# Performance work log

Measured on AMD Instinct MI355X. Metric: run time of the kernel, lower is better.

Reference implementation:

```python
import jax, jax.numpy as jnp
import numpy as np

D_MODEL = 1024
D_INNER = 2048   # expand=2
D_STATE = 16
D_CONV = 4
DT_RANK = 64     # ceil(d_model/16)
BATCH = 4
SEQLEN = 2048


def setup_inputs() -> dict:
    key = jax.random.key(0)
    ks = jax.random.split(key, 9)
    f = lambda k, shape, s=0.02: jax.random.normal(k, shape, dtype=jnp.float32) * s
    return {
        "x": jax.random.normal(ks[0], (BATCH, SEQLEN, D_MODEL), dtype=jnp.float32),
        "norm_w": jnp.ones((D_MODEL,), jnp.float32),
        "in_proj_w": f(ks[1], (2 * D_INNER, D_MODEL)),
        "conv_w": f(ks[2], (D_INNER, D_CONV), 0.1),
        "conv_b": f(ks[3], (D_INNER,), 0.1),
        "x_proj_w": f(ks[4], (DT_RANK + 2 * D_STATE, D_INNER)),
        "dt_proj_w": f(ks[5], (D_INNER, DT_RANK), 0.1),
        "dt_proj_b": f(ks[6], (D_INNER,), 0.1),
        "A_log": jnp.log(jnp.tile(jnp.arange(1, D_STATE + 1, dtype=jnp.float32), (D_INNER, 1))),
        "D_param": jnp.ones((D_INNER,), jnp.float32),
        "out_proj_w": f(ks[7], (D_MODEL, D_INNER)),
    }


def _rmsnorm(x, w):
    eps = jnp.finfo(jnp.float32).eps
    var = jnp.mean(x * x, axis=-1, keepdims=True)
    return x * jax.lax.rsqrt(var + eps) * w


def _mamba(x_norm, in_proj_w, conv_w, conv_b, x_proj_w,
           dt_proj_w, dt_proj_b, A_log, D_param, out_proj_w):
    B, L, _ = x_norm.shape
    # input projection -> [B, L, 2*D_INNER], split into x and gate z
    xz = jnp.einsum('bld,ed->ble', x_norm, in_proj_w)
    x_in, z = jnp.split(xz, 2, axis=-1)
    # causal depthwise conv1d (kernel D_CONV, left pad D_CONV-1)
    x_c = jax.lax.conv_general_dilated(
        x_in.transpose(0, 2, 1),                 # [B, D_INNER, L]
        conv_w[:, None, :],                      # [D_INNER, 1, D_CONV]
        window_strides=(1,), padding=[(D_CONV - 1, 0)],
        dimension_numbers=('NCH', 'OIH', 'NCH'),
        feature_group_count=D_INNER,
    ) + conv_b[None, :, None]
    u = jax.nn.silu(x_c.transpose(0, 2, 1))      # [B, L, D_INNER]
    # SSM parameters
    x_dbl = jnp.einsum('bld,ed->ble', u, x_proj_w)  # [B, L, DT_RANK+2*D_STATE]
    dt, B_mat, C_mat = jnp.split(x_dbl, [DT_RANK, DT_RANK + D_STATE], axis=-1)
    dt = jax.nn.softplus(jnp.einsum('blr,dr->bld', dt, dt_proj_w) + dt_proj_b)  # [B,L,D_INNER]
    A = -jnp.exp(A_log)                          # [D_INNER, D_STATE]

    # selective scan over time; state h: [B, D_INNER, D_STATE]
    def step(h, inputs):
        dt_t, B_t, C_t, u_t = inputs             # [B,Dn],[B,S],[B,S],[B,Dn]
        dA = jnp.exp(dt_t[:, :, None] * A)       # [B, Dn, S]
        h = dA * h + (dt_t * u_t)[:, :, None] * B_t[:, None, :]
        y_t = jnp.einsum('bds,bs->bd', h, C_t)
        return h, y_t

    h0 = jnp.zeros((B, D_INNER, D_STATE), x_norm.dtype)
    xs = (dt.transpose(1, 0, 2), B_mat.transpose(1, 0, 2),
          C_mat.transpose(1, 0, 2), u.transpose(1, 0, 2))
    _, ys = jax.lax.scan(step, h0, xs)           # [L, B, D_INNER]
    y = ys.transpose(1, 0, 2) + D_param * u
    y = y * jax.nn.silu(z)
    return jnp.einsum('bld,ed->ble', y, out_proj_w)  # [B, L, D_MODEL]


def reference(x, norm_w, in_proj_w, conv_w, conv_b, x_proj_w,
              dt_proj_w, dt_proj_b, A_log, D_param, out_proj_w):
    x_norm = _rmsnorm(x, norm_w)
    out = _mamba(x_norm, in_proj_w, conv_w, conv_b, x_proj_w,
                 dt_proj_w, dt_proj_b, A_log, D_param, out_proj_w)
    return x + out
```

## Files before the change

kernel.cpp:

```cpp
#include <hip/hip_runtime.h>
#include <hip/hip_bf16.h>
#include <math.h>

#define DM 1024
#define DI 2048
#define DS 16
#define DC 4
#define DR 64
#define NB 4
#define SL 2048
#define BL (NB * SL)
#define DXP (DR + 2 * DS)
#define NC 32
#define CL (SL / NC)

typedef __hip_bfloat16 bf16;
typedef __attribute__((ext_vector_type(8))) short short8;
typedef __attribute__((ext_vector_type(4))) float floatx4;
typedef unsigned int u32;

__device__ __forceinline__ float to_f(float v) { return v; }
__device__ __forceinline__ float to_f(bf16 v) { return __bfloat162float(v); }
template <typename T> __device__ __forceinline__ T from_f(float v);
template <> __device__ __forceinline__ float from_f<float>(float v) { return v; }
template <> __device__ __forceinline__ bf16 from_f<bf16>(float v) { return __float2bfloat16(v); }

__device__ __forceinline__ float bfbits2f(unsigned short u) {
  u32 b = ((u32)u) << 16;
  return __builtin_bit_cast(float, b);
}
__device__ __forceinline__ short f2bfbits(float v) {
  bf16 b = __float2bfloat16(v);
  return __builtin_bit_cast(short, b);
}
__device__ __forceinline__ float fsilu(float v) {
  return v * __builtin_amdgcn_rcpf(1.f + __expf(-v));
}

__device__ __forceinline__ void gload16(const ushort* g, ushort* l) {
  __builtin_amdgcn_global_load_lds((const __attribute__((address_space(1))) void*)g,
                                   (__attribute__((address_space(3))) void*)l,
                                   16, 0, 0);
}

__device__ __forceinline__ void vmw4() { asm volatile("s_waitcnt vmcnt(4)" ::: "memory"); }
__device__ __forceinline__ void vmw0() { asm volatile("s_waitcnt vmcnt(0)" ::: "memory"); }
__device__ __forceinline__ void barx() {
  asm volatile("" ::: "memory");
  __builtin_amdgcn_s_barrier();
  asm volatile("" ::: "memory");
}

__global__ __launch_bounds__(256) void f2b_k(const float* __restrict__ src,
                                             bf16* __restrict__ dst, int n) {
  int i = blockIdx.x * 256 + threadIdx.x;
  if (i < n) dst[i] = from_f<bf16>(src[i]);
}

__global__ __launch_bounds__(256) void rmsnorm_k(const float* __restrict__ x,
                                                 const float* __restrict__ w,
                                                 bf16* __restrict__ o) {
  int row = blockIdx.x;
  const float* xr = x + (size_t)row * DM;
  float ss = 0.f;
  for (int i = threadIdx.x; i < DM; i += 256) { float v = xr[i]; ss += v * v; }
  for (int off = 32; off > 0; off >>= 1) ss += __shfl_down(ss, off);
  __shared__ float sred[4];
  __shared__ float sscale;
  if ((threadIdx.x & 63) == 0) sred[threadIdx.x >> 6] = ss;
  __syncthreads();
  if (threadIdx.x == 0) {
    float t = sred[0] + sred[1] + sred[2] + sred[3];
    sscale = rsqrtf(t / (float)DM + 1.1920929e-7f);
  }
  __syncthreads();
  float sc = sscale;
  bf16* orow = o + (size_t)row * DM;
  for (int i = threadIdx.x; i < DM; i += 256) orow[i] = from_f<bf16>(xr[i] * sc * w[i]);
}

template <int MODE>
__global__ __launch_bounds__(512, 1) void gemm256(const bf16* __restrict__ A,
                                                  const bf16* __restrict__ W,
                                                  int M, int N, int K,
                                                  bf16* __restrict__ Cx,
                                                  bf16* __restrict__ Cz, int nsplit,
                                                  float* __restrict__ Cf,
                                                  const float* __restrict__ R) {
  __shared__ ushort SH[65536];
  const int tid = threadIdx.x;
  const int lane = tid & 63, wv = tid >> 6;
  const int wr = wv >> 2, wc = wv & 3;
  const int row15 = lane & 15, quad = lane >> 4;

  int ntm = M >> 8, ntn = N >> 8, nwg = ntm * ntn;
  int bid = blockIdx.x;
  int swz = (bid & 7) * (nwg >> 3) + (bid >> 3);
  int bm0 = (swz % ntm) << 8, bn0 = (swz / ntm) << 8;

  const int nt = K >> 6;
  const ushort* Au = (const ushort*)A;
  const ushort* Wu = (const ushort*)W;

  const int w4u = lane ^ (((lane >> 5) & 1) << 1);
  const int Wsw = (((row15 << 6) | (quad << 4)) ^ (((row15 >> 3) & 1) << 5));
  const char* SHb = (const char*)SH;
  const int Abase0 = (wr << 14) + Wsw;
  const int Abase1 = 32768 + (wr << 14) + Wsw;
  const int Bbase0 = 65536 + ((wc >> 1) << 14) + ((wc & 1) << 13) + Wsw;
  const int Bbase1 = Bbase0 + 32768;

  auto stageA = [&](int tt, int half, int buf) {
    const ushort* g = Au + (size_t)(bm0 + half * 128) * K + tt * 64;
    char* lds = (char*)SH + (size_t)(buf * 2 + half) * 16384;
#pragma unroll
    for (int i = 0; i < 2; ++i) {
      int sub = wv + i * 8;
      int r = ((sub >> 1) << 4) | (w4u >> 2);
      int ce = ((sub & 1) << 5) | ((w4u & 3) << 3);
      gload16(g + (size_t)r * K + ce, (ushort*)(lds + sub * 1024));
    }
  };
  auto stageB = [&](int tt, int half, int buf) {
    const ushort* g = Wu + (size_t)(bn0 + half * 128) * K + tt * 64;
    char* lds = (char*)SH + 65536 + (size_t)(buf * 2 + half) * 16384;
#pragma unroll
    for (int i = 0; i < 2; ++i) {
      int sub = wv + i * 8;
      int r = ((sub >> 1) << 4) | (w4u >> 2);
      int ce = ((sub & 1) << 5) | ((w4u & 3) << 3);
      gload16(g + (size_t)r * K + ce, (ushort*)(lds + sub * 1024));
    }
  };

  short8 a_f[4][2], bq[2][2][2];
  floatx4 acc[8][4] = {};

#define LDA_(base, mh) do { _Pragma("unroll") for (int mi = 0; mi < 4; ++mi) \
  { _Pragma("unroll") for (int kk = 0; kk < 2; ++kk) \
    a_f[mi][kk] = *(const short8*)(SHb + (base) + ((((mh)*4 + mi)*2 + kk) << 10)); } } while (0)
#define LDB_(base, nh) do { _Pragma("unroll") for (int ni = 0; ni < 2; ++ni) \
  { _Pragma("unroll") for (int kk = 0; kk < 2; ++kk) \
    bq[nh][ni][kk] = *(const short8*)(SHb + (base) + (((((nh)*2 + ni)*2 + kk)) << 10)); } } while (0)
#define MM_(mh, nh) do { __builtin_amdgcn_s_setprio(1); \
  _Pragma("unroll") for (int mi = 0; mi < 4; ++mi) \
  { _Pragma("unroll") for (int ni = 0; ni < 2; ++ni) \
    { _Pragma("unroll") for (int kk = 0; kk < 2; ++kk) \
      acc[(mh)*4+mi][(nh)*2+ni] = __builtin_amdgcn_mfma_f32_16x16x32_bf16( \
          a_f[mi][kk], bq[nh][ni][kk], acc[(mh)*4+mi][(nh)*2+ni], 0, 0, 0); } } \
  __builtin_amdgcn_s_setprio(0); } while (0)

#define TILE_(t, AB, BB, curbuf, nxtbuf) do { \
  int tp1 = (t) + 1, tp2 = (t) + 2; \
  LDA_(AB, 0); LDB_(BB, 0); \
  if (tp1 < nt) stageA(tp1, 0, nxtbuf); \
  barx(); MM_(0, 0); barx(); \
  LDB_(BB, 1); \
  if (tp1 < nt) stageA(tp1, 1, nxtbuf); \
  barx(); MM_(0, 1); barx(); \
  LDA_(AB, 1); \
  if (tp2 < nt) stageB(tp2, 0, curbuf); \
  barx(); MM_(1, 1); barx(); \
  if (tp2 < nt) stageB(tp2, 1, curbuf); \
  barx(); MM_(1, 0); \
  if (tp2 < nt) vmw4(); else vmw0(); \
  barx(); \
} while (0)

  stageB(0, 0, 0); stageB(0, 1, 0); stageA(0, 0, 0); stageA(0, 1, 0);
  stageB(1, 0, 1); stageB(1, 1, 1);
  vmw4();
  barx();

  for (int t = 0; t < nt; t += 2) {
    TILE_(t, Abase0, Bbase0, 0, 1);
    TILE_(t + 1, Abase1, Bbase1, 1, 0);
  }
#undef TILE_
#undef MM_
#undef LDB_
#undef LDA_

#pragma unroll
  for (int mi8 = 0; mi8 < 8; ++mi8) {
#pragma unroll
    for (int ni4 = 0; ni4 < 4; ++ni4) {
#pragma unroll
      for (int reg = 0; reg < 4; ++reg) {
        int grow = bm0 + wr * 128 + mi8 * 16 + quad * 4 + reg;
        int gcol = bn0 + wc * 64 + ni4 * 16 + row15;
        float v = acc[mi8][ni4][reg];
        if (MODE == 1) {
          if (gcol < nsplit) {
            Cx[(size_t)grow * DI + gcol] = from_f<bf16>(v);
          } else {
            Cz[(size_t)grow * DI + (gcol - nsplit)] = from_f<bf16>(fsilu(v));
          }
        } else {
          size_t o = (size_t)grow * N + gcol;
          Cf[o] = v + R[o];
        }
      }
    }
  }
}

#define TM 128
#define TN 128
#define TK 32
#define LDK 40
template <int MODE>
__global__ __launch_bounds__(256) void gemm_mfma(const bf16* __restrict__ A,
                                                 const bf16* __restrict__ W,
                                                 int M, int N, int K,
                                                 bf16* __restrict__ Cx,
                                                 bf16* __restrict__ Cz, int nsplit,
                                                 float* __restrict__ Cf,
                                                 const float* __restrict__ R,
                                                 const float* __restrict__ bias) {
  __shared__ ushort Asm[TM][TK];
  __shared__ ushort Bsm[TN][TK];
  int bm = blockIdx.y * TM, bn = blockIdx.x * TN;
  int tid = threadIdx.x;
  int lane = tid & 63, wave = tid >> 6;
  int wm = (wave & 1) * 64, wn = (wave >> 1) * 64;
  int row15 = lane & 15, quad = lane >> 4;

  int srow = lane >> 2;
  int scol = (lane & 3) * 8;
  int s0 = wave * 2, s1 = wave * 2 + 1;

  const ushort* Au = (const ushort*)A;
  const ushort* Wu = (const ushort*)W;
  const ushort* ag0 = Au + (size_t)(bm + s0 * 16 + srow) * K + scol;
  const ushort* ag1 = Au + (size_t)(bm + s1 * 16 + srow) * K + scol;
  const ushort* bg0 = Wu + (size_t)(bn + s0 * 16 + srow) * K + scol;
  const ushort* bg1 = Wu + (size_t)(bn + s1 * 16 + srow) * K + scol;
  ushort* la0 = &Asm[s0 * 16][0];
  ushort* la1 = &Asm[s1 * 16][0];
  ushort* lb0 = &Bsm[s0 * 16][0];
  ushort* lb1 = &Bsm[s1 * 16][0];

  floatx4 acc[4][4] = {};

  for (int k0 = 0; k0 < K; k0 += TK) {
    gload16(ag0 + k0, la0);
    gload16(ag1 + k0, la1);
    gload16(bg0 + k0, lb0);
    gload16(bg1 + k0, lb1);
    __syncthreads();
    short8 a_f[4], b_f[4];
#pragma unroll
    for (int i = 0; i < 4; ++i)
      a_f[i] = *(const short8*)&Asm[wm + i * 16 + row15][quad * 8];
#pragma unroll
    for (int j = 0; j < 4; ++j)
      b_f[j] = *(const short8*)&Bsm[wn + j * 16 + row15][quad * 8];
#pragma unroll
    for (int i = 0; i < 4; ++i)
#pragma unroll
      for (int j = 0; j < 4; ++j)
        acc[i][j] = __builtin_amdgcn_mfma_f32_16x16x32_bf16(a_f[i], b_f[j], acc[i][j], 0, 0, 0);
    __syncthreads();
  }
#pragma unroll
  for (int mi = 0; mi < 4; ++mi) {
#pragma unroll
    for (int ni = 0; ni < 4; ++ni) {
#pragma unroll
      for (int reg = 0; reg < 4; ++reg) {
        int grow = bm + wm + mi * 16 + quad * 4 + reg;
        int gcol = bn + wn + ni * 16 + row15;
        float v = acc[mi][ni][reg];
        if (MODE == 1) {
          if (gcol < nsplit) {
            Cx[(size_t)grow * DI + gcol] = from_f<bf16>(v);
          } else {
            Cz[(size_t)grow * DI + (gcol - nsplit)] = from_f<bf16>(fsilu(v));
          }
        } else if (MODE == 2) {
          size_t o = (size_t)grow * N + gcol;
          Cf[o] = v + R[o];
        } else {
          float t = v + bias[gcol];
          float sp = (t > 20.f) ? t : __logf(1.f + __expf(t));
          Cx[(size_t)grow * N + gcol] = from_f<bf16>(sp);
        }
      }
    }
  }
}

#define XKS 128
__global__ __launch_bounds__(256) void xproj_k(const bf16* __restrict__ u,
                                               const bf16* __restrict__ w,
                                               float* __restrict__ xdbl) {
  __shared__ ushort Asm[128][LDK];
  __shared__ ushort Bsm[96][LDK];
  int kbase = blockIdx.x * XKS;
  int bm = blockIdx.y * 128;
  int tid = threadIdx.x;
  int lane = tid & 63, wave = tid >> 6;
  int row15 = lane & 15, quad = lane >> 4;
  int srow = tid >> 1, skoff = (tid & 1) * 16;

  floatx4 acc[2][6] = {};
  const ushort* Au = (const ushort*)u;
  const ushort* Wu = (const ushort*)w;
  for (int k0 = kbase; k0 < kbase + XKS; k0 += TK) {
    const ushort* ag = Au + (size_t)(bm + srow) * DI + k0 + skoff;
    *(short8*)&Asm[srow][skoff]     = *(const short8*)ag;
    *(short8*)&Asm[srow][skoff + 8] = *(const short8*)(ag + 8);
    if (tid < 192) {
      const ushort* wg = Wu + (size_t)srow * DI + k0 + skoff;
      *(short8*)&Bsm[srow][skoff]     = *(const short8*)wg;
      *(short8*)&Bsm[srow][skoff + 8] = *(const short8*)(wg + 8);
    }
    __syncthreads();
    short8 a_f[2], b_f[6];
#pragma unroll
    for (int i = 0; i < 2; ++i)
      a_f[i] = *(const short8*)&Asm[wave * 32 + i * 16 + row15][quad * 8];
#pragma unroll
    for (int j = 0; j < 6; ++j)
      b_f[j] = *(const short8*)&Bsm[j * 16 + row15][quad * 8];
#pragma unroll
    for (int i = 0; i < 2; ++i)
#pragma unroll
      for (int j = 0; j < 6; ++j)
        acc[i][j] = __builtin_amdgcn_mfma_f32_16x16x32_bf16(a_f[i], b_f[j], acc[i][j], 0, 0, 0);
    __syncthreads();
  }
#pragma unroll
  for (int mi = 0; mi < 2; ++mi)
#pragma unroll
    for (int nj = 0; nj < 6; ++nj)
#pragma unroll
      for (int reg = 0; reg < 4; ++reg) {
        int grow = bm + wave * 32 + mi * 16 + quad * 4 + reg;
        int gcol = nj * 16 + row15;
        atomicAdd(&xdbl[(size_t)grow * DXP + gcol], acc[mi][nj][reg]);
      }
}

__global__ __launch_bounds__(256) void dtex_k(const float* __restrict__ xdbl,
                                              bf16* __restrict__ dtin) {
  int i = blockIdx.x * 256 + threadIdx.x;
  int r = i >> 6, c = i & 63;
  dtin[i] = from_f<bf16>(xdbl[(size_t)r * DXP + c]);
}

#define TSTRIP 8
__global__ __launch_bounds__(256) void conv_silu_k(const bf16* __restrict__ xin,
                                                   const float* __restrict__ cw,
                                                   const float* __restrict__ cb,
                                                   bf16* __restrict__ u) {
  int blk = blockIdx.x;
  int b = blk >> 8;
  int l0 = (blk & 255) * TSTRIP;
  int c0 = threadIdx.x * 8;

  float4 cw4[8];
  const float4* cwp = (const float4*)cw;
#pragma unroll
  for (int j = 0; j < 8; ++j) cw4[j] = cwp[c0 + j];
  float cbv[8];
  {
    float4 cb0 = *(const float4*)&cb[c0];
    float4 cb1 = *(const float4*)&cb[c0 + 4];
    cbv[0] = cb0.x; cbv[1] = cb0.y; cbv[2] = cb0.z; cbv[3] = cb0.w;
    cbv[4] = cb1.x; cbv[5] = cb1.y; cbv[6] = cb1.z; cbv[7] = cb1.w;
  }

  const ushort* base = (const ushort*)xin + ((size_t)(b * SL + l0) * DI + c0);
  ushort* ubase = (ushort*)u + ((size_t)(b * SL + l0) * DI + c0);

  short8 zz = {};
  short8 w0 = zz, w1 = zz, w2 = zz;
  if (l0 >= 3) {
    w0 = *(const short8*)(base - 3 * DI);
    w1 = *(const short8*)(base - 2 * DI);
    w2 = *(const short8*)(base - 1 * DI);
  }
#pragma unroll
  for (int l = 0; l < TSTRIP; ++l) {
    short8 w3 = *(const short8*)(base + (ptrdiff_t)l * DI);
    short8 outv;
#pragma unroll
    for (int j = 0; j < 8; ++j) {
      float a = cbv[j]
              + bfbits2f((unsigned short)w0[j]) * cw4[j].x
              + bfbits2f((unsigned short)w1[j]) * cw4[j].y
              + bfbits2f((unsigned short)w2[j]) * cw4[j].z
              + bfbits2f((unsigned short)w3[j]) * cw4[j].w;
      outv[j] = f2bfbits(fsilu(a));
    }
    *(short8*)(ubase + (ptrdiff_t)l * DI) = outv;
    w0 = w1; w1 = w2; w2 = w3;
  }
}

__global__ __launch_bounds__(256) void scan_p1(const bf16* __restrict__ dts,
                                               const bf16* __restrict__ u,
                                               const float* __restrict__ xdbl,
                                               const float* __restrict__ A_log,
                                               float* __restrict__ Pbuf,
                                               float* __restrict__ Qbuf) {
  int bid = blockIdx.x;
  int b = bid >> 8;
  int c = (bid >> 3) & (NC - 1);
  int d = (bid & 7) * 256 + threadIdx.x;

  float A[DS], h[DS], P[DS];
#pragma unroll
  for (int s = 0; s < DS; ++s) {
    A[s] = -__expf(A_log[d * DS + s]);
    h[s] = 0.f; P[s] = 1.f;
  }
  size_t bl0 = (size_t)b * SL + c * CL;
  size_t base = bl0 * DI + d;
  size_t xb = bl0 * DXP + DR;
  for (int l = 0; l < CL; ++l) {
    float dtv = to_f(dts[base]);
    float uv = to_f(u[base]);
    float du = dtv * uv;
#pragma unroll
    for (int s = 0; s < DS; ++s) {
      float Bv = xdbl[xb + s];
      float dA = __expf(dtv * A[s]);
      h[s] = dA * h[s] + du * Bv;
      P[s] *= dA;
    }
    base += DI;
    xb += DXP;
  }
  size_t o = ((size_t)(b * NC + c) * DS) * DI + d;
#pragma unroll
  for (int s = 0; s < DS; ++s) {
    Pbuf[o + (size_t)s * DI] = P[s];
    Qbuf[o + (size_t)s * DI] = h[s];
  }
}

__global__ __launch_bounds__(256) void scan_p2(float* __restrict__ Pbuf,
                                               float* __restrict__ Qbuf) {
  int bid = blockIdx.x;
  int b = bid >> 7;
  int s = (bid >> 3) & (DS - 1);
  int d = (bid & 7) * 256 + threadIdx.x;
  float h = 0.f;
  for (int c = 0; c < NC; ++c) {
    size_t idx = ((size_t)((b * NC + c) * DS + s)) * DI + d;
    float Pv = Pbuf[idx];
    float qv = Qbuf[idx];
    Qbuf[idx] = h;
    h = Pv * h + qv;
  }
}

__global__ __launch_bounds__(256) void scan_p3(const bf16* __restrict__ dts,
                                               bf16* __restrict__ u,
                                               const float* __restrict__ xdbl,
                                               const float* __restrict__ A_log,
                                               const float* __restrict__ Dp,
                                               const bf16* __restrict__ g,
                                               const float* __restrict__ Qbuf) {
  int bid = blockIdx.x;
  int b = bid >> 8;
  int c = (bid >> 3) & (NC - 1);
  int d = (bid & 7) * 256 + threadIdx.x;

  float A[DS], h[DS];
  size_t o = ((size_t)(b * NC + c) * DS) * DI + d;
#pragma unroll
  for (int s = 0; s < DS; ++s) {
    A[s] = -__expf(A_log[d * DS + s]);
    h[s] = Qbuf[o + (size_t)s * DI];
  }
  float Dd = Dp[d];
  size_t bl0 = (size_t)b * SL + c * CL;
  size_t base = bl0 * DI + d;
  size_t xb = bl0 * DXP + DR;
  for (int l = 0; l < CL; ++l) {
    float dtv = to_f(dts[base]);
    float uv = to_f(u[base]);
    float gv = to_f(g[base]);
    float du = dtv * uv;
    float p0 = 0.f, p1 = 0.f, p2 = 0.f, p3 = 0.f;
#pragma unroll
    for (int s = 0; s < DS; s += 4) {
      float dA0 = __expf(dtv * A[s + 0]);
      float dA1 = __expf(dtv * A[s + 1]);
      float dA2 = __expf(dtv * A[s + 2]);
      float dA3 = __expf(dtv * A[s + 3]);
      h[s + 0] = dA0 * h[s + 0] + du * xdbl[xb + s + 0];
      h[s + 1] = dA1 * h[s + 1] + du * xdbl[xb + s + 1];
      h[s + 2] = dA2 * h[s + 2] + du * xdbl[xb + s + 2];
      h[s + 3] = dA3 * h[s + 3] + du * xdbl[xb + s + 3];
      p0 += h[s + 0] * xdbl[xb + DS + s + 0];
      p1 += h[s + 1] * xdbl[xb + DS + s + 1];
      p2 += h[s + 2] * xdbl[xb + DS + s + 2];
      p3 += h[s + 3] * xdbl[xb + DS + s + 3];
    }
    float yv = ((p0 + p1) + (p2 + p3)) + Dd * uv;
    u[base] = from_f<bf16>(yv * gv);
    base += DI;
    xb += DXP;
  }
}

extern "C" void kernel_launch(void* const* d_in, const int* in_sizes, int n_in,
                              void* d_out, int out_size, void* d_ws, size_t ws_size,
                              hipStream_t stream) {
  const float* x        = (const float*)d_in[0];
  const float* norm_w   = (const float*)d_in[1];
  const float* in_projw = (const float*)d_in[2];
  const float* conv_w   = (const float*)d_in[3];
  const float* conv_b   = (const float*)d_in[4];
  const float* x_projw  = (const float*)d_in[5];
  const float* dt_projw = (const float*)d_in[6];
  const float* dt_projb = (const float*)d_in[7];
  const float* A_log    = (const float*)d_in[8];
  const float* Dp       = (const float*)d_in[9];
  const float* out_projw= (const float*)d_in[10];
  float* out = (float*)d_out;

  char* wsb = (char*)d_ws;
  bf16* x_buf  = (bf16*)wsb;
  bf16* z_buf  = (bf16*)(wsb + (size_t)BL * DI * 2);
  bf16* u_buf  = (bf16*)(wsb + (size_t)BL * DI * 4);
  char* ovl    = wsb + (size_t)BL * DI * 6;
  bf16* ipw_bf = (bf16*)ovl;
  float* xdbl   = (float*)ovl;
  bf16*  xpw_bf = (bf16*)(ovl + 3145728);
  bf16*  dtw_bf = (bf16*)(ovl + 3538944);
  bf16*  dtin_bf= (bf16*)(ovl + 3801088);
  bf16* xnorm_bf = u_buf;
  bf16* dt_buf   = x_buf;
  bf16* opw_bf   = x_buf;
  float* Pbuf = out;
  float* Qbuf = out + (size_t)NB * NC * DS * DI;

  f2b_k<<<(2 * DI * DM) / 256, 256, 0, stream>>>(in_projw, ipw_bf, 2 * DI * DM);
  rmsnorm_k<<<BL, 256, 0, stream>>>(x, norm_w, xnorm_bf);
  gemm256<1><<<(BL / 256) * (2 * DI / 256), 512, 0, stream>>>(
      xnorm_bf, ipw_bf, BL, 2 * DI, DM, x_buf, z_buf, DI, nullptr, nullptr);
  conv_silu_k<<<NB * (SL / TSTRIP), 256, 0, stream>>>(x_buf, conv_w, conv_b, u_buf);
  hipMemsetAsync(xdbl, 0, (size_t)BL * DXP * sizeof(float), stream);
  f2b_k<<<(DXP * DI + 255) / 256, 256, 0, stream>>>(x_projw, xpw_bf, DXP * DI);
  f2b_k<<<(DI * DR) / 256, 256, 0, stream>>>(dt_projw, dtw_bf, DI * DR);
  xproj_k<<<dim3(DI / XKS, BL / 128), 256, 0, stream>>>(u_buf, xpw_bf, xdbl);
  dtex_k<<<(BL * DR) / 256, 256, 0, stream>>>(xdbl, dtin_bf);
  gemm_mfma<3><<<dim3(DI / TN, BL / TM), 256, 0, stream>>>(
      dtin_bf, dtw_bf, BL, DI, DR, dt_buf, nullptr, 0, nullptr, nullptr, dt_projb);
  scan_p1<<<NB * NC * (DI / 256), 256, 0, stream>>>(dt_buf, u_buf, xdbl, A_log, Pbuf, Qbuf);
  scan_p2<<<NB * DS * (DI / 256), 256, 0, stream>>>(Pbuf, Qbuf);
  scan_p3<<<NB * NC * (DI / 256), 256, 0, stream>>>(dt_buf, u_buf, xdbl, A_log, Dp, z_buf, Qbuf);
  f2b_k<<<(DM * DI) / 256, 256, 0, stream>>>(out_projw, opw_bf, DM * DI);
  gemm256<2><<<(BL / 256) * (DM / 256), 512, 0, stream>>>(
      u_buf, opw_bf, BL, DM, DI, nullptr, nullptr, 0, out, x);
}
```

Baseline: 489.2 us.

## Add 256x128 ping-pong pipelined MFMA GEMM for output projection

Adds a new GEMM kernel with 256x128 tiles, K-step 64, and double-buffered LDS loaded through global_load_lds. MFMA work is interleaved with LDS fragment loads and raises wave priority during MFMA. The out_proj GEMM now uses it in place of the 256x256 kernel. The grid doubles, which raises CU occupancy for the M=8192, N=1024 shape, at the cost of reading the A operand more often and more barriers per tile.

```diff
diff --git a/kernel.cpp b/kernel.cpp
--- a/kernel.cpp
+++ b/kernel.cpp
@@ -44,6 +44,7 @@
 }
 
 __device__ __forceinline__ void vmw4() { asm volatile("s_waitcnt vmcnt(4)" ::: "memory"); }
+__device__ __forceinline__ void vmw2() { asm volatile("s_waitcnt vmcnt(2)" ::: "memory"); }
 __device__ __forceinline__ void vmw0() { asm volatile("s_waitcnt vmcnt(0)" ::: "memory"); }
 __device__ __forceinline__ void barx() {
   asm volatile("" ::: "memory");
@@ -198,6 +199,130 @@
           }
         } else {
           size_t o = (size_t)grow * N + gcol;
+          Cf[o] = v + R[o];
+        }
+      }
+    }
+  }
+}
+
+template <int MODE>
+__global__ __launch_bounds__(512, 1) void gemm_np(const bf16* __restrict__ A,
+                                                  const bf16* __restrict__ W,
+                                                  int M, int N, int K,
+                                                  bf16* __restrict__ Cx,
+                                                  bf16* __restrict__ Cz, int nsplit,
+                                                  float* __restrict__ Cf,
+                                                  const float* __restrict__ R) {
+  __shared__ ushort SH[49152];
+  const int tid = threadIdx.x;
+  const int lane = tid & 63, wv = tid >> 6;
+  const int wr = wv >> 1, wc = wv & 1;
+  const int row15 = lane & 15, quad = lane >> 4;
+
+  int ntm = M >> 8, ntn = N >> 7, nwg = ntm * ntn;
+  int bid = blockIdx.x;
+  int swz = (bid & 7) * (nwg >> 3) + (bid >> 3);
+  int bm0 = (swz % ntm) << 8, bn0 = (swz / ntm) << 7;
+
+  const int nt = K >> 6;
+  const ushort* Au = (const ushort*)A;
+  const ushort* Wu = (const ushort*)W;
+  const ushort* Ag = Au + (u32)bm0 * (u32)K;
+  const ushort* Bg = Wu + (u32)bn0 * (u32)K;
+
+  const int w4u = lane ^ (((lane >> 5) & 1) << 1);
+  const int sub0 = wv, sub1 = wv + 8;
+  const int r0 = ((sub0 >> 1) << 4) | (w4u >> 2);
+  const int c0 = ((sub0 & 1) << 5) | ((w4u & 3) << 3);
+  const int r1 = ((sub1 >> 1) << 4) | (w4u >> 2);
+  const int c1 = ((sub1 & 1) << 5) | ((w4u & 3) << 3);
+  ushort* shA = (ushort*)SH;
+  ushort* shB = (ushort*)SH + 32768;
+
+  auto stage = [&](const ushort* gbase, int rowoff, int tt, ushort* lbase) {
+    gload16(gbase + (u32)(rowoff + r0) * (u32)K + (u32)(tt * 64 + c0), lbase + (sub0 << 9));
+    gload16(gbase + (u32)(rowoff + r1) * (u32)K + (u32)(tt * 64 + c1), lbase + (sub1 << 9));
+  };
+
+  const int Wsw = (((row15 << 6) | (quad << 4)) ^ (((row15 >> 3) & 1) << 5));
+  const char* SHb = (const char*)SH;
+  const int AB0 = (wr << 13) + Wsw;
+  const int AB1 = 32768 + AB0;
+  const int BB0 = 65536 + (wc << 13) + Wsw;
+  const int BB1 = BB0 + 16384;
+
+  short8 a0[2][2], a1[2][2], bq0A[2][2], bq0B[2][2], bq1[2][2];
+  floatx4 acc[4][4] = {};
+
+#define LDA_(dst, base, mh) do { _Pragma("unroll") for (int i_ = 0; i_ < 2; ++i_) \
+  { _Pragma("unroll") for (int kk = 0; kk < 2; ++kk) \
+    dst[i_][kk] = *(const short8*)(SHb + (base) + ((((mh)*2 + i_)*2 + kk) << 10)); } } while (0)
+#define LDB_(dst, base, nh) do { _Pragma("unroll") for (int j_ = 0; j_ < 2; ++j_) \
+  { _Pragma("unroll") for (int kk = 0; kk < 2; ++kk) \
+    dst[j_][kk] = *(const short8*)(SHb + (base) + ((((nh)*2 + j_)*2 + kk) << 10)); } } while (0)
+#define MM_(aset, bset, mh, nh) do { __builtin_amdgcn_s_setprio(1); \
+  _Pragma("unroll") for (int i_ = 0; i_ < 2; ++i_) \
+  { _Pragma("unroll") for (int j_ = 0; j_ < 2; ++j_) \
+    { _Pragma("unroll") for (int kk = 0; kk < 2; ++kk) \
+      acc[(mh)*2+i_][(nh)*2+j_] = __builtin_amdgcn_mfma_f32_16x16x32_bf16( \
+          aset[i_][kk], bset[j_][kk], acc[(mh)*2+i_][(nh)*2+j_], 0, 0, 0); } } \
+  __builtin_amdgcn_s_setprio(0); } while (0)
+
+#define TILE_(t, ABc, BBc, ABn, BBn, BQU, BQF, CURB, NXTB) do { \
+  int tp1 = (t) + 1, tp2 = (t) + 2; \
+   \
+  LDB_(bq1, BBc, 1); \
+  if (tp1 < nt) stage(Ag, 0, tp1, shA + (NXTB) * 16384); \
+  barx(); MM_(a0, BQU, 0, 0); barx(); \
+   \
+  LDA_(a1, ABc, 1); \
+  if (tp1 < nt) stage(Ag, 128, tp1, shA + (NXTB) * 16384 + 8192); \
+  barx(); MM_(a0, bq1, 0, 1); barx(); \
+   \
+  if (tp2 < nt) stage(Bg, 0, tp2, shB + (CURB) * 8192); \
+  barx(); MM_(a1, bq1, 1, 1); \
+  if (tp2 < nt) vmw2(); else vmw0(); \
+  barx(); \
+   \
+  if (tp1 < nt) { LDA_(a0, ABn, 0); LDB_(BQF, BBn, 0); } \
+  barx(); MM_(a1, BQU, 1, 0); barx(); \
+} while (0)
+
+  stage(Bg, 0, 0, shB);
+  stage(Ag, 0, 0, shA);
+  stage(Ag, 128, 0, shA + 8192);
+  if (nt > 1) { stage(Bg, 0, 1, shB + 8192); vmw2(); } else { vmw0(); }
+  barx();
+  LDA_(a0, AB0, 0);
+  LDB_(bq0A, BB0, 0);
+
+  for (int t = 0; t < nt; t += 2) {
+    TILE_(t,     AB0, BB0, AB1, BB1, bq0A, bq0B, 0, 1);
+    TILE_(t + 1, AB1, BB1, AB0, BB0, bq0B, bq0A, 1, 0);
+  }
+#undef TILE_
+#undef MM_
+#undef LDB_
+#undef LDA_
+
+#pragma unroll
+  for (int mi = 0; mi < 4; ++mi) {
+#pragma unroll
+    for (int ni = 0; ni < 4; ++ni) {
+#pragma unroll
+      for (int reg = 0; reg < 4; ++reg) {
+        int grow = bm0 + wr * 64 + mi * 16 + quad * 4 + reg;
+        int gcol = bn0 + wc * 64 + ni * 16 + row15;
+        float v = acc[mi][ni][reg];
+        if (MODE == 1) {
+          if (gcol < nsplit) {
+            Cx[(u32)grow * DI + (u32)gcol] = from_f<bf16>(v);
+          } else {
+            Cz[(u32)grow * DI + (u32)(gcol - nsplit)] = from_f<bf16>(fsilu(v));
+          }
+        } else {
+          u32 o = (u32)grow * (u32)N + (u32)gcol;
           Cf[o] = v + R[o];
         }
       }
@@ -557,6 +682,6 @@
   scan_p2<<<NB * DS * (DI / 256), 256, 0, stream>>>(Pbuf, Qbuf);
   scan_p3<<<NB * NC * (DI / 256), 256, 0, stream>>>(dt_buf, u_buf, xdbl, A_log, Dp, z_buf, Qbuf);
   f2b_k<<<(DM * DI) / 256, 256, 0, stream>>>(out_projw, opw_bf, DM * DI);
-  gemm256<2><<<(BL / 256) * (DM / 256), 512, 0, stream>>>(
+  gemm_np<2><<<(BL / 256) * (DM / 128), 512, 0, stream>>>(
       u_buf, opw_bf, BL, DM, DI, nullptr, nullptr, 0, out, x);
 }
```

After: 466.0 us. 1.05x faster.
